# Optimization experiments

Hardware: AMD Instinct MI355X
Metric: run time of the kernel (lower is better)

The kernel has to match this reference:

```python
import jax, jax.numpy as jnp
import numpy as np

B, T, V, H = 32, 256, 16, 256


def _layer_norm(x, g, b, eps=1e-5):
    m = jnp.mean(x, axis=-1, keepdims=True)
    v = jnp.mean(jnp.square(x - m), axis=-1, keepdims=True)
    return (x - m) * jax.lax.rsqrt(v + eps) * g + b


def setup_inputs() -> dict:
    keys = iter(jax.random.split(jax.random.key(0), 16))

    def nrm(shape, s=0.02):
        return (jax.random.normal(next(keys), shape, dtype=jnp.float32) * s).astype(jnp.float32)

    return {
        "x": nrm((B, T, V, H), 1.0),
        "context": nrm((B, T, H), 1.0),
        "joint_Wa": nrm((V * H, H)),
        "joint_ba": jnp.zeros((H,), jnp.float32),
        "joint_Wc": nrm((H, H)),
        "joint_Wi": nrm((H, H)),
        "joint_bi": jnp.zeros((H,), jnp.float32),
        "joint_Wglu": nrm((H, 2 * V)),
        "joint_bglu": jnp.zeros((2 * V,), jnp.float32),
        "joint_Wskip": nrm((V * H, V)),
        "joint_bskip": jnp.zeros((V,), jnp.float32),
        "joint_ln_g": jnp.ones((V,), jnp.float32),
        "joint_ln_b": jnp.zeros((V,), jnp.float32),
        "var_Wa": nrm((V, H, H)),
        "var_ba": jnp.zeros((V, H), jnp.float32),
        "var_Wi": nrm((V, H, H)),
        "var_bi": jnp.zeros((V, H), jnp.float32),
        "var_Wglu": nrm((V, H, 2 * H)),
        "var_bglu": jnp.zeros((V, 2 * H), jnp.float32),
        "var_ln_g": jnp.ones((V, H), jnp.float32),
        "var_ln_b": jnp.zeros((V, H), jnp.float32),
    }


def reference(x, context, joint_Wa, joint_ba, joint_Wc, joint_Wi, joint_bi,
              joint_Wglu, joint_bglu, joint_Wskip, joint_bskip,
              joint_ln_g, joint_ln_b,
              var_Wa, var_ba, var_Wi, var_bi, var_Wglu, var_bglu,
              var_ln_g, var_ln_b):
    b, t, v, h = x.shape
    Xi = x.reshape(b, t, v * h)  # flatten last two dims

    # ---- joint GRN (with context) producing variable logits [b,t,v] ----
    a = Xi @ joint_Wa + joint_ba + context @ joint_Wc
    a = jax.nn.elu(a)
    i = a @ joint_Wi + joint_bi
    g = i @ joint_Wglu + joint_bglu
    g1, g2 = jnp.split(g, 2, axis=-1)  # GLU: first half gated by sigmoid(second)
    glu_out = g1 * jax.nn.sigmoid(g2)
    skip = Xi @ joint_Wskip + joint_bskip  # out_size != in_size -> skip projection
    sparse_weights = jax.nn.softmax(_layer_norm(glu_out + skip, joint_ln_g, joint_ln_b), axis=-1)

    # ---- per-variable GRNs, batched over the variable axis ----
    av = jax.nn.elu(jnp.einsum('btvh,vhk->btvk', x, var_Wa) + var_ba)
    iv = jnp.einsum('btvh,vhk->btvk', av, var_Wi) + var_bi
    gv = jnp.einsum('btvh,vhd->btvd', iv, var_Wglu) + var_bglu
    gv1, gv2 = jnp.split(gv, 2, axis=-1)
    tv = _layer_norm(gv1 * jax.nn.sigmoid(gv2) + x, var_ln_g, var_ln_b)  # [b,t,v,h]

    # stack(dim=-1) + matmul with weights == weighted sum over variables
    variable_ctx = jnp.einsum('btvh,btv->bth', tv, sparse_weights)
    return variable_ctx, sparse_weights
```

## Files before the change

### kernel.cpp

```cpp
#include <hip/hip_runtime.h>

typedef unsigned short u16;
typedef __attribute__((ext_vector_type(8))) __bf16 bf16x8;
typedef __attribute__((ext_vector_type(4))) float f32x4;
typedef __attribute__((ext_vector_type(8))) u16 u16x8;

__device__ __forceinline__ u16 f2b(float f) {
  union { float f; unsigned u; } v; v.f = f;
  return (u16)((v.u + 0x7fffu + ((v.u >> 16) & 1u)) >> 16);
}
__device__ __forceinline__ float b2f(u16 h) {
  union { unsigned u; float f; } v; v.u = ((unsigned)h) << 16;
  return v.f;
}
__device__ __forceinline__ f32x4 mfma16(bf16x8 a, bf16x8 b, f32x4 c) {
  return __builtin_amdgcn_mfma_f32_16x16x32_bf16(a, b, c, 0, 0, 0);
}
__device__ __forceinline__ void gl_lds16(const void* g, void* l) {
  __builtin_amdgcn_global_load_lds(
      (const __attribute__((address_space(1))) void*)g,
      (__attribute__((address_space(3))) void*)l, 16, 0, 0);
}
__device__ __forceinline__ u16x8 cvt8(float4 a, float4 b) {
  u16x8 o;
  o[0] = f2b(a.x); o[1] = f2b(a.y); o[2] = f2b(a.z); o[3] = f2b(a.w);
  o[4] = f2b(b.x); o[5] = f2b(b.y); o[6] = f2b(b.z); o[7] = f2b(b.w);
  return o;
}

__global__ __launch_bounds__(256) void transpose_cast(
    const float* __restrict__ src, u16* __restrict__ dst,
    int R, int C, int dstStride, long srcBatch, long dstBatch)
{
  __shared__ float tile[32][33];
  src += (long)blockIdx.z * srcBatch;
  dst += (long)blockIdx.z * dstBatch;
  const int c0 = blockIdx.x * 32, r0 = blockIdx.y * 32;
  const int tx = threadIdx.x & 31, ty = threadIdx.x >> 5;
  for (int i = ty; i < 32; i += 8) {
    int r = r0 + i, cc = c0 + tx;
    if (r < R && cc < C) tile[i][tx] = src[(long)r * C + cc];
  }
  __syncthreads();
  for (int i = ty; i < 32; i += 8) {
    int cc = c0 + i, r = r0 + tx;
    if (cc < C && r < R) dst[(long)cc * dstStride + r] = f2b(tile[tx][i]);
  }
}

__global__ __launch_bounds__(256) void var_w_prep(
    const float* __restrict__ W, u16* __restrict__ dstbase, int rbase)
{
  const int v = blockIdx.x;
  const int kc = blockIdx.y;
  const int n = threadIdx.x;
  const float* src = W + (size_t)v * 65536 + (size_t)kc * 64 * 256 + n;
  u16* dst = dstbase + (size_t)v * 262144 + (size_t)(rbase + kc) * 16384;
#pragma unroll
  for (int l = 0; l < 8; ++l) {
    u16x8 o;
#pragma unroll
    for (int e = 0; e < 8; ++e) o[e] = f2b(src[(l * 8 + e) * 256]);
    const int chunk = n * 8 + (l ^ (n & 7));
    *(u16x8*)&dst[chunk * 8] = o;
  }
}

__global__ __launch_bounds__(256) void var_wglu_prep(
    const float* __restrict__ W, u16* __restrict__ dstbase)
{
  const int v = blockIdx.x;
  const int kc = blockIdx.y;
  u16* dst = dstbase + (size_t)v * 262144 + (size_t)(8 + kc) * 16384;
#pragma unroll
  for (int half = 0; half < 2; ++half) {
    const int n = threadIdx.x + half * 256;
    const float* src = W + (size_t)v * 131072 + (size_t)kc * 32 * 512 + n;
    const int s = n >> 1;
#pragma unroll
    for (int l = 0; l < 4; ++l) {
      u16x8 o;
#pragma unroll
      for (int e = 0; e < 8; ++e) o[e] = f2b(src[(l * 8 + e) * 512]);
      const int chunk = s * 8 + ((((n & 1) * 4 + l)) ^ (s & 7));
      *(u16x8*)&dst[chunk * 8] = o;
    }
  }
}

#define K1TOT 4352
__global__ __launch_bounds__(256, 3) void gemm1(
    const float* __restrict__ x, const float* __restrict__ ctx,
    const u16* __restrict__ bt1, const float* __restrict__ ba,
    const float* __restrict__ bskip, u16* __restrict__ a_bf, float* __restrict__ skip_f)
{
  __shared__ u16 As[32 * 64];
  __shared__ u16 Bs[288 * 64];
  const int tid = threadIdx.x;
  const int n0 = blockIdx.x * 32;
  const int w = tid >> 6, lane = tid & 63;
  const int q = lane >> 4, c = lane & 15;
  const int rt = w & 1, cg = w >> 1;
  const int t0 = cg ? 9 : 0;
  const int nt = cg ? 8 : 9;

  f32x4 acc[9];
#pragma unroll
  for (int i = 0; i < 9; ++i) acc[i] = f32x4{0.f, 0.f, 0.f, 0.f};

  const int sr = tid >> 3, sp = tid & 7;
  const int sl = sp ^ (sr & 7);

  for (int kb = 0; kb < K1TOT; kb += 64) {
    {
      const float* s = (kb < 4096)
          ? (x + (size_t)(n0 + sr) * 4096 + kb + sl * 8)
          : (ctx + (size_t)(n0 + sr) * 256 + (kb - 4096) + sl * 8);
      float4 v0 = ((const float4*)s)[0];
      float4 v1 = ((const float4*)s)[1];
      *(u16x8*)&As[tid * 8] = cvt8(v0, v1);
    }
#pragma unroll
    for (int i = 0; i < 9; ++i) {
      const int cb = (i * 4 + w) * 64;
      const int cid = cb + lane;
      const int row = cid >> 3, p = cid & 7;
      const int l = p ^ (row & 7);
      const u16* src = (row < 272) ? (bt1 + (size_t)row * K1TOT + kb + l * 8) : bt1;
      gl_lds16(src, &Bs[cb * 8]);
    }
    __syncthreads();
#pragma unroll
    for (int kk = 0; kk < 2; ++kk) {
      const int arow = rt * 16 + c;
      bf16x8 af = *(const bf16x8*)&As[(arow * 64 + kk * 32 + q * 8) ^ ((arow & 7) << 3)];
#pragma unroll
      for (int ti = 0; ti < 9; ++ti) {
        if (ti < nt) {
          const int n16 = (t0 + ti) * 16 + c;
          bf16x8 bfr = *(const bf16x8*)&Bs[(n16 * 64 + kk * 32 + q * 8) ^ ((n16 & 7) << 3)];
          acc[ti] = mfma16(af, bfr, acc[ti]);
        }
      }
    }
    __syncthreads();
  }
#pragma unroll
  for (int ti = 0; ti < 9; ++ti) {
    if (ti < nt) {
      const int col = (t0 + ti) * 16 + c;
#pragma unroll
      for (int j = 0; j < 4; ++j) {
        const long n = n0 + rt * 16 + q * 4 + j;
        float vv = acc[ti][j];
        if (col < 256) {
          vv += ba[col];
          vv = vv > 0.f ? vv : expm1f(vv);
          a_bf[n * 256 + col] = f2b(vv);
        } else {
          skip_f[n * 16 + (col - 256)] = vv + bskip[col - 256];
        }
      }
    }
  }
}

__global__ __launch_bounds__(256, 3) void gemm_i(
    const u16* __restrict__ a_bf, const u16* __restrict__ wiT,
    const float* __restrict__ bi, u16* __restrict__ i_bf)
{
  __shared__ u16 As[32 * 64];
  __shared__ u16 Bs[256 * 64];
  const int tid = threadIdx.x;
  const int n0 = blockIdx.x * 32;
  const int w = tid >> 6, lane = tid & 63;
  const int q = lane >> 4, c = lane & 15;
  const int rt = w & 1, cg = w >> 1;

  f32x4 acc[8];
#pragma unroll
  for (int i = 0; i < 8; ++i) acc[i] = f32x4{0.f, 0.f, 0.f, 0.f};

  for (int kb = 0; kb < 256; kb += 64) {
    {
      const int row = tid >> 3, p = tid & 7;
      const int l = p ^ (row & 7);
      gl_lds16(a_bf + (size_t)(n0 + row) * 256 + kb + l * 8, &As[w * 512]);
    }
#pragma unroll
    for (int i = 0; i < 8; ++i) {
      const int cb = (i * 4 + w) * 64;
      const int cid = cb + lane;
      const int row = cid >> 3, p = cid & 7;
      const int l = p ^ (row & 7);
      gl_lds16(wiT + (size_t)row * 256 + kb + l * 8, &Bs[cb * 8]);
    }
    __syncthreads();
#pragma unroll
    for (int kk = 0; kk < 2; ++kk) {
      const int arow = rt * 16 + c;
      bf16x8 af = *(const bf16x8*)&As[(arow * 64 + kk * 32 + q * 8) ^ ((arow & 7) << 3)];
#pragma unroll
      for (int ti = 0; ti < 8; ++ti) {
        const int n16 = (cg * 8 + ti) * 16 + c;
        bf16x8 bfr = *(const bf16x8*)&Bs[(n16 * 64 + kk * 32 + q * 8) ^ ((n16 & 7) << 3)];
        acc[ti] = mfma16(af, bfr, acc[ti]);
      }
    }
    __syncthreads();
  }
#pragma unroll
  for (int ti = 0; ti < 8; ++ti) {
    const int col = (cg * 8 + ti) * 16 + c;
    const float bb = bi[col];
#pragma unroll
    for (int j = 0; j < 4; ++j) {
      const long n = n0 + rt * 16 + q * 4 + j;
      i_bf[n * 256 + col] = f2b(acc[ti][j] + bb);
    }
  }
}

__global__ __launch_bounds__(256) void joint_tail(
    const u16* __restrict__ i_bf, const u16* __restrict__ wgluT,
    const float* __restrict__ bglu, const float* __restrict__ skip_f,
    const float* __restrict__ lng, const float* __restrict__ lnb,
    float* __restrict__ swout)
{
  __shared__ float wlds[32 * 257];
  __shared__ float ilds[4][256];
  const int tid = threadIdx.x;
  for (int jj = 0; jj < 32; ++jj) wlds[jj * 257 + tid] = b2f(wgluT[jj * 256 + tid]);
  const int w = tid >> 6, lane = tid & 63;
  const long n = (long)blockIdx.x * 4 + w;
  {
    const u16* src = i_bf + n * 256 + lane * 4;
    float4 f;
    f.x = b2f(src[0]); f.y = b2f(src[1]); f.z = b2f(src[2]); f.w = b2f(src[3]);
    *(float4*)&ilds[w][lane * 4] = f;
  }
  __syncthreads();
  const int cc32 = lane & 31;
  const int k0 = (lane >> 5) * 128;
  float acc = 0.f;
  for (int k = 0; k < 128; ++k) acc += ilds[w][k0 + k] * wlds[cc32 * 257 + k0 + k];
  acc += __shfl_xor(acc, 32, 64);
  const float gfull = acc + bglu[cc32];
  const int cc = lane & 15;
  const float g1 = __shfl(gfull, cc, 64);
  const float g2 = __shfl(gfull, cc + 16, 64);
  const float glu = g1 / (1.f + __expf(-g2));
  const float y = glu + skip_f[n * 16 + cc];
  float s = y, ss = y * y;
#pragma unroll
  for (int d = 1; d < 16; d <<= 1) { s += __shfl_xor(s, d, 64); ss += __shfl_xor(ss, d, 64); }
  const float m = s * (1.f / 16.f);
  const float var = ss * (1.f / 16.f) - m * m;
  const float t = (y - m) * rsqrtf(var + 1e-5f) * lng[cc] + lnb[cc];
  float mx = t;
#pragma unroll
  for (int d = 1; d < 16; d <<= 1) mx = fmaxf(mx, __shfl_xor(mx, d, 64));
  const float e = __expf(t - mx);
  float es = e;
#pragma unroll
  for (int d = 1; d < 16; d <<= 1) es += __shfl_xor(es, d, 64);
  if (lane < 16) swout[n * 16 + lane] = e / es;
}

__global__ __launch_bounds__(1024, 1) void var_chain(
    const float* __restrict__ x, const u16* __restrict__ varw,
    const float* __restrict__ vba, const float* __restrict__ vbi,
    const float* __restrict__ vbglu, const float* __restrict__ vlng,
    const float* __restrict__ vlnb, const float* __restrict__ sw,
    float* __restrict__ out)
{
  extern __shared__ u16 smem[];
  u16* const xt1 = smem;
  u16* const wtb = smem + 32768;
  float* const red   = (float*)(smem + 65536);
  float* const muinv = red + 1024;

  const int tid = threadIdx.x;
  const int w = tid >> 6, lane = tid & 63;
  const int q = lane >> 4, c = lane & 15;
  const int rt = w >> 2, cg = w & 3;
  const int vbase = blockIdx.x * 4;
  const int n0 = blockIdx.y * 128;

  f32x4 outacc[2][4];
#pragma unroll
  for (int p = 0; p < 2; ++p)
#pragma unroll
    for (int u = 0; u < 4; ++u) outacc[p][u] = f32x4{0.f, 0.f, 0.f, 0.f};

  auto STAGE = [&](int b, int tn) {
    const u16* tb = varw + (size_t)(vbase + (tn >> 4)) * 262144 + (size_t)(tn & 15) * 16384;
    u16* dst = wtb + (b << 14);
#pragma unroll
    for (int i = 0; i < 2; ++i) {
      const int cb = (i * 16 + w) * 64;
      gl_lds16(tb + (size_t)(cb + lane) * 8, dst + (size_t)cb * 8);
    }
  };

  int cur = 0;
  STAGE(0, 0);

  for (int vi = 0; vi < 4; ++vi) {
    const int v = vbase + vi;
    const int tb0 = vi * 16;

#pragma unroll
    for (int jj = 0; jj < 4; ++jj) {
      const int cid = jj * 1024 + tid;
      const int r = cid >> 5, p = cid & 31;
      const int l = (p & 24) | ((p & 7) ^ (r & 7));
      const float* s = x + (size_t)(n0 + r) * 4096 + (size_t)v * 256 + l * 8;
      float4 v0 = ((const float4*)s)[0];
      float4 v1 = ((const float4*)s)[1];
      *(u16x8*)&xt1[cid * 8] = cvt8(v0, v1);
    }
    __syncthreads();

    f32x4 acc2[2][4];
#pragma unroll
    for (int p = 0; p < 2; ++p)
#pragma unroll
      for (int ti = 0; ti < 4; ++ti) acc2[p][ti] = f32x4{0.f, 0.f, 0.f, 0.f};

    for (int t = tb0; t < tb0 + 4; ++t) {
      const int tn = t + 1 < 64 ? t + 1 : 63;
      STAGE(cur ^ 1, tn);
      const u16* wcur = wtb + (cur << 14);
      const int kc = t - tb0;
#pragma unroll
      for (int kk = 0; kk < 2; ++kk) {
        bf16x8 a[2];
#pragma unroll
        for (int p = 0; p < 2; ++p) {
          const int r = (rt * 2 + p) * 16 + c;
          a[p] = *(const bf16x8*)&xt1[(r * 256 + kc * 64 + kk * 32 + q * 8) ^ ((r & 7) << 3)];
        }
#pragma unroll
        for (int ti = 0; ti < 4; ++ti) {
          const int n16 = (cg * 4 + ti) * 16 + c;
          bf16x8 b = *(const bf16x8*)&wcur[(n16 * 64 + kk * 32 + q * 8) ^ ((n16 & 7) << 3)];
          acc2[0][ti] = mfma16(a[0], b, acc2[0][ti]);
          acc2[1][ti] = mfma16(a[1], b, acc2[1][ti]);
        }
      }
      __syncthreads();
      cur ^= 1;
    }
#pragma unroll
    for (int p = 0; p < 2; ++p)
#pragma unroll
      for (int ti = 0; ti < 4; ++ti) {
        const int col = (cg * 4 + ti) * 16 + c;
        const float bb = vba[v * 256 + col];
#pragma unroll
        for (int j = 0; j < 4; ++j) {
          const int row = (rt * 2 + p) * 16 + q * 4 + j;
          float vv = acc2[p][ti][j] + bb;
          vv = vv > 0.f ? vv : expm1f(vv);
          xt1[(row * 256 + col) ^ ((row & 7) << 3)] = f2b(vv);
        }
      }
    __syncthreads();

#pragma unroll
    for (int p = 0; p < 2; ++p)
#pragma unroll
      for (int ti = 0; ti < 4; ++ti) acc2[p][ti] = f32x4{0.f, 0.f, 0.f, 0.f};
    for (int t = tb0 + 4; t < tb0 + 8; ++t) {
      const int tn = t + 1 < 64 ? t + 1 : 63;
      STAGE(cur ^ 1, tn);
      const u16* wcur = wtb + (cur << 14);
      const int kc = t - (tb0 + 4);
#pragma unroll
      for (int kk = 0; kk < 2; ++kk) {
        bf16x8 a[2];
#pragma unroll
        for (int p = 0; p < 2; ++p) {
          const int r = (rt * 2 + p) * 16 + c;
          a[p] = *(const bf16x8*)&xt1[(r * 256 + kc * 64 + kk * 32 + q * 8) ^ ((r & 7) << 3)];
        }
#pragma unroll
        for (int ti = 0; ti < 4; ++ti) {
          const int n16 = (cg * 4 + ti) * 16 + c;
          bf16x8 b = *(const bf16x8*)&wcur[(n16 * 64 + kk * 32 + q * 8) ^ ((n16 & 7) << 3)];
          acc2[0][ti] = mfma16(a[0], b, acc2[0][ti]);
          acc2[1][ti] = mfma16(a[1], b, acc2[1][ti]);
        }
      }
      __syncthreads();
      cur ^= 1;
    }
#pragma unroll
    for (int p = 0; p < 2; ++p)
#pragma unroll
      for (int ti = 0; ti < 4; ++ti) {
        const int col = (cg * 4 + ti) * 16 + c;
        const float bb = vbi[v * 256 + col];
#pragma unroll
        for (int j = 0; j < 4; ++j) {
          const int row = (rt * 2 + p) * 16 + q * 4 + j;
          xt1[(row * 256 + col) ^ ((row & 7) << 3)] = f2b(acc2[p][ti][j] + bb);
        }
      }
    __syncthreads();

    f32x4 acc3[2][8];
#pragma unroll
    for (int p = 0; p < 2; ++p)
#pragma unroll
      for (int u = 0; u < 8; ++u) acc3[p][u] = f32x4{0.f, 0.f, 0.f, 0.f};
    for (int t = tb0 + 8; t < tb0 + 16; ++t) {
      const int tn = t + 1 < 64 ? t + 1 : 63;
      STAGE(cur ^ 1, tn);
      const u16* wcur = wtb + (cur << 14);
      const int kc = t - (tb0 + 8);
      bf16x8 a[2];
#pragma unroll
      for (int p = 0; p < 2; ++p) {
        const int r = (rt * 2 + p) * 16 + c;
        a[p] = *(const bf16x8*)&xt1[(r * 256 + kc * 32 + q * 8) ^ ((r & 7) << 3)];
      }
#pragma unroll
      for (int u = 0; u < 8; ++u) {
        const int ct = cg * 4 + (u & 3) + ((u >> 2) << 4);
        const int n = ct * 16 + c;
        const int idx = (n >> 1) * 64 + ((((n & 1) * 4 + q) ^ ((n >> 1) & 7)) * 8);
        bf16x8 b = *(const bf16x8*)&wcur[idx];
        acc3[0][u] = mfma16(a[0], b, acc3[0][u]);
        acc3[1][u] = mfma16(a[1], b, acc3[1][u]);
      }
      __syncthreads();
      cur ^= 1;
    }

    float b1v[4], b2v[4], lgv[4], lbv[4];
#pragma unroll
    for (int u = 0; u < 4; ++u) {
      const int col = cg * 64 + u * 16 + c;
      b1v[u] = vbglu[v * 512 + col];
      b2v[u] = vbglu[v * 512 + 256 + col];
      lgv[u] = vlng[v * 256 + col];
      lbv[u] = vlnb[v * 256 + col];
    }
    float rs[2][4], rss[2][4];
#pragma unroll
    for (int p = 0; p < 2; ++p)
#pragma unroll
      for (int j = 0; j < 4; ++j) { rs[p][j] = 0.f; rss[p][j] = 0.f; }
#pragma unroll
    for (int p = 0; p < 2; ++p)
#pragma unroll
      for (int u = 0; u < 4; ++u) {
        const int col = cg * 64 + u * 16 + c;
#pragma unroll
        for (int j = 0; j < 4; ++j) {
          const int row = (rt * 2 + p) * 16 + q * 4 + j;
          const float g1 = acc3[p][u][j] + b1v[u];
          const float g2 = acc3[p][u + 4][j] + b2v[u];
          const float glu = g1 / (1.f + __expf(-g2));
          const float r = glu + x[(size_t)(n0 + row) * 4096 + (size_t)v * 256 + col];
          acc3[p][u][j] = r;
          rs[p][j] += r; rss[p][j] += r * r;
        }
      }
#pragma unroll
    for (int p = 0; p < 2; ++p)
#pragma unroll
      for (int j = 0; j < 4; ++j)
#pragma unroll
        for (int d = 1; d < 16; d <<= 1) {
          rs[p][j]  += __shfl_xor(rs[p][j], d, 64);
          rss[p][j] += __shfl_xor(rss[p][j], d, 64);
        }
    if (c == 0) {
#pragma unroll
      for (int p = 0; p < 2; ++p)
#pragma unroll
        for (int j = 0; j < 4; ++j) {
          const int row = (rt * 2 + p) * 16 + q * 4 + j;
          red[row * 8 + cg * 2]     = rs[p][j];
          red[row * 8 + cg * 2 + 1] = rss[p][j];
        }
    }
    __syncthreads();
    if (tid < 128) {
      float ms = 0.f, vs = 0.f;
#pragma unroll
      for (int ww = 0; ww < 4; ++ww) { ms += red[tid * 8 + ww * 2]; vs += red[tid * 8 + ww * 2 + 1]; }
      const float mm = ms * (1.f / 256.f);
      muinv[tid * 2]     = mm;
      muinv[tid * 2 + 1] = rsqrtf(vs * (1.f / 256.f) - mm * mm + 1e-5f);
    }
    __syncthreads();
#pragma unroll
    for (int p = 0; p < 2; ++p) {
#pragma unroll
      for (int j = 0; j < 4; ++j) {
        const int row = (rt * 2 + p) * 16 + q * 4 + j;
        const float mu = muinv[row * 2], inv = muinv[row * 2 + 1];
        const float wv = sw[(size_t)(n0 + row) * 16 + v];
#pragma unroll
        for (int u = 0; u < 4; ++u) {
          const float tv = (acc3[p][u][j] - mu) * inv * lgv[u] + lbv[u];
          outacc[p][u][j] += tv * wv;
        }
      }
    }
    __syncthreads();
  }

#pragma unroll
  for (int p = 0; p < 2; ++p)
#pragma unroll
    for (int u = 0; u < 4; ++u) {
      const int col = cg * 64 + u * 16 + c;
#pragma unroll
      for (int j = 0; j < 4; ++j) {
        const int row = (rt * 2 + p) * 16 + q * 4 + j;
        atomicAdd(&out[(size_t)(n0 + row) * 256 + col], outacc[p][u][j]);
      }
    }
}

extern "C" void kernel_launch(void* const* d_in, const int* in_sizes, int n_in,
                              void* d_out, int out_size, void* d_ws, size_t ws_size,
                              hipStream_t stream) {
  const float* x     = (const float*)d_in[0];
  const float* ctx   = (const float*)d_in[1];
  const float* jWa   = (const float*)d_in[2];
  const float* jba   = (const float*)d_in[3];
  const float* jWc   = (const float*)d_in[4];
  const float* jWi   = (const float*)d_in[5];
  const float* jbi   = (const float*)d_in[6];
  const float* jWglu = (const float*)d_in[7];
  const float* jbglu = (const float*)d_in[8];
  const float* jWskip= (const float*)d_in[9];
  const float* jbskip= (const float*)d_in[10];
  const float* jlng  = (const float*)d_in[11];
  const float* jlnb  = (const float*)d_in[12];
  const float* vWa   = (const float*)d_in[13];
  const float* vba   = (const float*)d_in[14];
  const float* vWi   = (const float*)d_in[15];
  const float* vbi   = (const float*)d_in[16];
  const float* vWglu = (const float*)d_in[17];
  const float* vbglu = (const float*)d_in[18];
  const float* vlng  = (const float*)d_in[19];
  const float* vlnb  = (const float*)d_in[20];
  float* out = (float*)d_out;

  char* ws = (char*)d_ws;
  size_t off = 0;
  auto alloc = [&](size_t bytes) { void* p = ws + off; off += (bytes + 255) & ~(size_t)255; return p; };
  u16* bt1     = (u16*)alloc((size_t)272 * 4352 * 2);
  u16* wiT     = (u16*)alloc((size_t)256 * 256 * 2);
  u16* wgluT   = (u16*)alloc((size_t)32 * 256 * 2);
  u16* varw    = (u16*)alloc((size_t)16 * 262144 * 2);
  u16* a_bf    = (u16*)alloc((size_t)8192 * 256 * 2);
  u16* i_bf    = (u16*)alloc((size_t)8192 * 256 * 2);
  float* skipf = (float*)alloc((size_t)8192 * 16 * 4);

  hipMemsetAsync(bt1, 0, (size_t)272 * 4352 * 2, stream);
  hipMemsetAsync(out, 0, (size_t)8192 * 256 * 4, stream);

  dim3 blk(256);
  transpose_cast<<<dim3(8, 128, 1),  blk, 0, stream>>>(jWa,   bt1,              4096, 256, 4352, 0, 0);
  transpose_cast<<<dim3(8, 8, 1),    blk, 0, stream>>>(jWc,   bt1 + 4096,       256,  256, 4352, 0, 0);
  transpose_cast<<<dim3(1, 128, 1),  blk, 0, stream>>>(jWskip,bt1 + 256 * 4352, 4096, 16,  4352, 0, 0);
  transpose_cast<<<dim3(8, 8, 1),    blk, 0, stream>>>(jWi,   wiT,   256, 256, 256, 0, 0);
  transpose_cast<<<dim3(1, 8, 1),    blk, 0, stream>>>(jWglu, wgluT, 256, 32,  256, 0, 0);
  var_w_prep<<<dim3(16, 4), blk, 0, stream>>>(vWa, varw, 0);
  var_w_prep<<<dim3(16, 4), blk, 0, stream>>>(vWi, varw, 4);
  var_wglu_prep<<<dim3(16, 8), blk, 0, stream>>>(vWglu, varw);

  gemm1<<<dim3(256), blk, 0, stream>>>(x, ctx, bt1, jba, jbskip, a_bf, skipf);
  gemm_i<<<dim3(256), blk, 0, stream>>>(a_bf, wiT, jbi, i_bf);
  joint_tail<<<dim3(2048), blk, 0, stream>>>(i_bf, wgluT, jbglu, skipf, jlng, jlnb,
                                             out + (size_t)8192 * 256);

  hipFuncSetAttribute((const void*)var_chain, hipFuncAttributeMaxDynamicSharedMemorySize, 136192);
  var_chain<<<dim3(4, 64), dim3(1024), 136192, stream>>>(x, varw, vba, vbi, vbglu,
                                                         vlng, vlnb,
                                                         out + (size_t)8192 * 256, out);
}
```

Baseline: 479.3 us.

## Deepen weight-tile prefetch to two stages with explicit vmcnt waits and setprio

```diff
diff --git a/kernel.cpp b/kernel.cpp
--- a/kernel.cpp
+++ b/kernel.cpp
@@ -302,14 +302,7 @@
       gl_lds16(tb + (size_t)(cb + lane) * 8, dst + (size_t)cb * 8);
     }
   };
-
-  int cur = 0;
-  STAGE(0, 0);
-
-  for (int vi = 0; vi < 4; ++vi) {
-    const int v = vbase + vi;
-    const int tb0 = vi * 16;
-
+  auto XSTAGE = [&](int v) {
 #pragma unroll
     for (int jj = 0; jj < 4; ++jj) {
       const int cid = jj * 1024 + tid;
@@ -320,7 +313,27 @@
       float4 v1 = ((const float4*)s)[1];
       *(u16x8*)&xt1[cid * 8] = cvt8(v0, v1);
     }
-    __syncthreads();
+  };
+
+  auto ROUND_TAIL = [&](int t) {
+    __builtin_amdgcn_s_barrier();
+    __builtin_amdgcn_sched_barrier(0);
+    STAGE(t & 1, (t + 2 < 64) ? t + 2 : 63);
+    __builtin_amdgcn_sched_barrier(0);
+    asm volatile("s_waitcnt vmcnt(2)" ::: "memory");
+    __builtin_amdgcn_sched_barrier(0);
+    __builtin_amdgcn_s_barrier();
+    __builtin_amdgcn_sched_barrier(0);
+  };
+
+  STAGE(0, 0);
+  STAGE(1, 1);
+  XSTAGE(vbase);
+  __syncthreads();
+
+  int t = 0;
+  for (int vi = 0; vi < 4; ++vi) {
+    const int v = vbase + vi;
 
     f32x4 acc2[2][4];
 #pragma unroll
@@ -328,11 +341,9 @@
 #pragma unroll
       for (int ti = 0; ti < 4; ++ti) acc2[p][ti] = f32x4{0.f, 0.f, 0.f, 0.f};
 
-    for (int t = tb0; t < tb0 + 4; ++t) {
-      const int tn = t + 1 < 64 ? t + 1 : 63;
-      STAGE(cur ^ 1, tn);
-      const u16* wcur = wtb + (cur << 14);
-      const int kc = t - tb0;
+    for (int kc = 0; kc < 4; ++kc, ++t) {
+      const u16* wcur = wtb + ((t & 1) << 14);
+      __builtin_amdgcn_s_setprio(1);
 #pragma unroll
       for (int kk = 0; kk < 2; ++kk) {
         bf16x8 a[2];
@@ -349,8 +360,8 @@
           acc2[1][ti] = mfma16(a[1], b, acc2[1][ti]);
         }
       }
-      __syncthreads();
-      cur ^= 1;
+      __builtin_amdgcn_s_setprio(0);
+      ROUND_TAIL(t);
     }
 #pragma unroll
     for (int p = 0; p < 2; ++p)
@@ -372,11 +383,9 @@
     for (int p = 0; p < 2; ++p)
 #pragma unroll
       for (int ti = 0; ti < 4; ++ti) acc2[p][ti] = f32x4{0.f, 0.f, 0.f, 0.f};
-    for (int t = tb0 + 4; t < tb0 + 8; ++t) {
-      const int tn = t + 1 < 64 ? t + 1 : 63;
-      STAGE(cur ^ 1, tn);
-      const u16* wcur = wtb + (cur << 14);
-      const int kc = t - (tb0 + 4);
+    for (int kc = 0; kc < 4; ++kc, ++t) {
+      const u16* wcur = wtb + ((t & 1) << 14);
+      __builtin_amdgcn_s_setprio(1);
 #pragma unroll
       for (int kk = 0; kk < 2; ++kk) {
         bf16x8 a[2];
@@ -393,8 +402,8 @@
           acc2[1][ti] = mfma16(a[1], b, acc2[1][ti]);
         }
       }
-      __syncthreads();
-      cur ^= 1;
+      __builtin_amdgcn_s_setprio(0);
+      ROUND_TAIL(t);
     }
 #pragma unroll
     for (int p = 0; p < 2; ++p)
@@ -415,17 +424,15 @@
     for (int p = 0; p < 2; ++p)
 #pragma unroll
       for (int u = 0; u < 8; ++u) acc3[p][u] = f32x4{0.f, 0.f, 0.f, 0.f};
-    for (int t = tb0 + 8; t < tb0 + 16; ++t) {
-      const int tn = t + 1 < 64 ? t + 1 : 63;
-      STAGE(cur ^ 1, tn);
-      const u16* wcur = wtb + (cur << 14);
-      const int kc = t - (tb0 + 8);
+    for (int kc = 0; kc < 8; ++kc, ++t) {
+      const u16* wcur = wtb + ((t & 1) << 14);
       bf16x8 a[2];
 #pragma unroll
       for (int p = 0; p < 2; ++p) {
         const int r = (rt * 2 + p) * 16 + c;
         a[p] = *(const bf16x8*)&xt1[(r * 256 + kc * 32 + q * 8) ^ ((r & 7) << 3)];
       }
+      __builtin_amdgcn_s_setprio(1);
 #pragma unroll
       for (int u = 0; u < 8; ++u) {
         const int ct = cg * 4 + (u & 3) + ((u >> 2) << 4);
@@ -435,8 +442,8 @@
         acc3[0][u] = mfma16(a[0], b, acc3[0][u]);
         acc3[1][u] = mfma16(a[1], b, acc3[1][u]);
       }
-      __syncthreads();
-      cur ^= 1;
+      __builtin_amdgcn_s_setprio(0);
+      ROUND_TAIL(t);
     }
 
     float b1v[4], b2v[4], lgv[4], lbv[4];
@@ -513,6 +520,10 @@
       }
     }
     __syncthreads();
+    if (vi < 3) {
+      XSTAGE(v + 1);
+      __syncthreads();
+    }
   }
 
 #pragma unroll
```

After: 475.8 us. No clear change (-0.7%).
